# Optimization experiments

Hardware: AMD Instinct MI355X
Metric: run time of the kernel (lower is better)

Reference implementation:

```python
import jax, jax.numpy as jnp
import numpy as np

N = 1048576   # samples
C = 64        # classes (Y unique targets)
S = 8         # subgroups


def setup_inputs() -> dict:
    key = jax.random.key(0)
    k1, k2, k3 = jax.random.split(key, 3)
    logits = jax.random.normal(k1, (N, C), dtype=jnp.float32)
    targets = jax.random.randint(k2, (N,), 0, C, dtype=jnp.int64)
    subgroup_inf = jax.random.randint(k3, (N,), 0, S, dtype=jnp.int64)
    return {"logits": logits, "targets": targets, "subgroup_inf": subgroup_inf}


def reference(logits, targets, subgroup_inf):
    # per-sample cross-entropy (loss_fn with reduction='none')
    logp = jax.nn.log_softmax(logits, axis=-1)                       # [N, C]
    per_sample = -jnp.take_along_axis(logp, targets[:, None], axis=-1)[:, 0]  # [N]

    # composite (target, subgroup) key -> group counts via one scatter-add
    key_ids = targets * S + subgroup_inf                              # [N]
    counts = jax.ops.segment_sum(jnp.ones_like(per_sample), key_ids,
                                 num_segments=C * S)                  # [C*S]
    # every sample's own group has count >= 1, so no div-by-zero
    weighted = per_sample / counts[key_ids]
    return jnp.sum(weighted)
```

## Files before the change

### kernel.cpp

```cpp
#include <hip/hip_runtime.h>


#define NKEYS 512
#define NSLICES 512
typedef float v4f __attribute__((ext_vector_type(4)));

__device__ __forceinline__ float pick4(v4f v, int j) {
    float r = v.x;
    r = (j == 1) ? v.y : r;
    r = (j == 2) ? v.z : r;
    r = (j == 3) ? v.w : r;
    return r;
}

__device__ __forceinline__ float esum4(v4f v) {
    return __expf(v.x) + __expf(v.y) + __expf(v.z) + __expf(v.w);
}

__global__ __launch_bounds__(256)
void orl_hist_kernel(const float* __restrict__ logits,
                     const int* __restrict__ targets,
                     const int* __restrict__ subg,
                     float* __restrict__ psum,
                     unsigned int* __restrict__ pcnt,
                     int n) {
    __shared__ float        lsum[NKEYS];
    __shared__ unsigned int lcnt[NKEYS];
    for (int i = threadIdx.x; i < NKEYS; i += 256) { lsum[i] = 0.0f; lcnt[i] = 0u; }
    __syncthreads();

    const int lane = threadIdx.x & 63;
    const int q    = lane & 15;
    const int g    = lane >> 4;
    const int wave = (blockIdx.x << 2) | (threadIdx.x >> 6);
    const int nwaves = gridDim.x << 2;

    int base = wave * 16;
    for (; base + 16 <= n; base += nwaves * 16) {
        const int r0 = base + g, r1 = base + 4 + g, r2 = base + 8 + g, r3 = base + 12 + g;
        const v4f v0 = __builtin_nontemporal_load((const v4f*)(logits + (size_t)r0 * 64) + q);
        const v4f v1 = __builtin_nontemporal_load((const v4f*)(logits + (size_t)r1 * 64) + q);
        const v4f v2 = __builtin_nontemporal_load((const v4f*)(logits + (size_t)r2 * 64) + q);
        const v4f v3 = __builtin_nontemporal_load((const v4f*)(logits + (size_t)r3 * 64) + q);
        const int t0 = targets[r0], t1 = targets[r1], t2 = targets[r2], t3 = targets[r3];
        const int u0 = subg[r0],    u1 = subg[r1],    u2 = subg[r2],    u3 = subg[r3];

        float s0 = esum4(v0), s1 = esum4(v1), s2 = esum4(v2), s3 = esum4(v3);
        #pragma unroll
        for (int m = 1; m < 16; m <<= 1) {
            s0 += __shfl_xor(s0, m, 16);
            s1 += __shfl_xor(s1, m, 16);
            s2 += __shfl_xor(s2, m, 16);
            s3 += __shfl_xor(s3, m, 16);
        }
        if ((t0 >> 2) == q) {
            const float ps = __logf(s0) - pick4(v0, t0 & 3);
            atomicAdd(&lsum[t0 * 8 + u0], ps); atomicAdd(&lcnt[t0 * 8 + u0], 1u);
        }
        if ((t1 >> 2) == q) {
            const float ps = __logf(s1) - pick4(v1, t1 & 3);
            atomicAdd(&lsum[t1 * 8 + u1], ps); atomicAdd(&lcnt[t1 * 8 + u1], 1u);
        }
        if ((t2 >> 2) == q) {
            const float ps = __logf(s2) - pick4(v2, t2 & 3);
            atomicAdd(&lsum[t2 * 8 + u2], ps); atomicAdd(&lcnt[t2 * 8 + u2], 1u);
        }
        if ((t3 >> 2) == q) {
            const float ps = __logf(s3) - pick4(v3, t3 & 3);
            atomicAdd(&lsum[t3 * 8 + u3], ps); atomicAdd(&lcnt[t3 * 8 + u3], 1u);
        }
    }
    for (int o = 0; o < 16; o += 4) {
        const int r = base + o + g;
        if (r < n) {
            const v4f v = *((const v4f*)(logits + (size_t)r * 64) + q);
            const int t = targets[r];
            float s = esum4(v);
            #pragma unroll
            for (int m = 1; m < 16; m <<= 1) s += __shfl_xor(s, m, 16);
            if ((t >> 2) == q) {
                const float ps = __logf(s) - pick4(v, t & 3);
                const int key = t * 8 + subg[r];
                atomicAdd(&lsum[key], ps); atomicAdd(&lcnt[key], 1u);
            }
        }
    }

    __syncthreads();
    const size_t sbase = (size_t)blockIdx.x * NKEYS;
    for (int i = threadIdx.x; i < NKEYS; i += 256) {
        psum[sbase + i] = lsum[i];
        pcnt[sbase + i] = lcnt[i];
    }
}

__global__ __launch_bounds__(1024)
void orl_reduce_kernel(const float* __restrict__ psum,
                       const unsigned int* __restrict__ pcnt,
                       float* __restrict__ out) {
    const int t = threadIdx.x;
    const int k = t & (NKEYS - 1);
    const int h = t >> 9;
    float s = 0.0f; unsigned int c = 0u;
    const int b0 = h * (NSLICES / 2);
    #pragma unroll 8
    for (int b = b0; b < b0 + NSLICES / 2; ++b) {
        s += psum[(size_t)b * NKEYS + k];
        c += pcnt[(size_t)b * NKEYS + k];
    }
    __shared__ float        s2[NKEYS];
    __shared__ unsigned int c2[NKEYS];
    if (h) { s2[k] = s; c2[k] = c; }
    __syncthreads();
    float v = 0.0f;
    if (!h) {
        const float S = s + s2[k];
        const unsigned int C = c + c2[k];
        v = C ? S / (float)C : 0.0f;
    }
    #pragma unroll
    for (int m = 32; m > 0; m >>= 1) v += __shfl_down(v, m, 64);
    __shared__ float wred[16];
    if ((t & 63) == 0) wred[t >> 6] = v;
    __syncthreads();
    if (t == 0) {
        float r = 0.0f;
        #pragma unroll
        for (int w = 0; w < 16; ++w) r += wred[w];
        out[0] = r;
    }
}

extern "C" void kernel_launch(void* const* d_in, const int* in_sizes, int n_in,
                              void* d_out, int out_size, void* d_ws, size_t ws_size,
                              hipStream_t stream) {
    const float* logits  = (const float*)d_in[0];
    const int*   targets = (const int*)d_in[1];
    const int*   subg    = (const int*)d_in[2];
    const int n = in_sizes[1];
    float* out = (float*)d_out;

    float*        psum = (float*)d_ws;
    unsigned int* pcnt = (unsigned int*)((char*)d_ws + (size_t)NSLICES * NKEYS * 4);

    orl_hist_kernel<<<NSLICES, 256, 0, stream>>>(logits, targets, subg, psum, pcnt, n);
    orl_reduce_kernel<<<1, 1024, 0, stream>>>(psum, pcnt, out);
}
```

Measured before the change: 373.2 us.

## Vectorize target/subgroup loads and spread final reduction over 64 blocks

In the histogram kernel, each 16-lane group now handles four consecutive rows, so targets and subgroups come in with one int4 load each instead of scalar loads. The logits loads also become per-row contiguous for each group. The reduce kernel moves from a single 1024-thread block to 64 blocks of 256 threads, each summing 8 keys across slices, with shuffle and shared reductions and a final atomicAdd into an output zeroed by a memset. This targets the serial single-block reduce and the scattered index loads, at the cost of an extra memset launch and nondeterministic float atomic ordering.

```diff
diff --git a/kernel.cpp b/kernel.cpp
--- a/kernel.cpp
+++ b/kernel.cpp
@@ -37,13 +37,14 @@
 
     int base = wave * 16;
     for (; base + 16 <= n; base += nwaves * 16) {
-        const int r0 = base + g, r1 = base + 4 + g, r2 = base + 8 + g, r3 = base + 12 + g;
-        const v4f v0 = __builtin_nontemporal_load((const v4f*)(logits + (size_t)r0 * 64) + q);
-        const v4f v1 = __builtin_nontemporal_load((const v4f*)(logits + (size_t)r1 * 64) + q);
-        const v4f v2 = __builtin_nontemporal_load((const v4f*)(logits + (size_t)r2 * 64) + q);
-        const v4f v3 = __builtin_nontemporal_load((const v4f*)(logits + (size_t)r3 * 64) + q);
-        const int t0 = targets[r0], t1 = targets[r1], t2 = targets[r2], t3 = targets[r3];
-        const int u0 = subg[r0],    u1 = subg[r1],    u2 = subg[r2],    u3 = subg[r3];
+        const int r0 = base + g * 4;
+        const int4 t4 = *(const int4*)(targets + r0);
+        const int4 u4 = *(const int4*)(subg + r0);
+        const float* rowp = logits + (size_t)r0 * 64 + q * 4;
+        const v4f v0 = __builtin_nontemporal_load((const v4f*)(rowp));
+        const v4f v1 = __builtin_nontemporal_load((const v4f*)(rowp + 64));
+        const v4f v2 = __builtin_nontemporal_load((const v4f*)(rowp + 128));
+        const v4f v3 = __builtin_nontemporal_load((const v4f*)(rowp + 192));
 
         float s0 = esum4(v0), s1 = esum4(v1), s2 = esum4(v2), s3 = esum4(v3);
         #pragma unroll
@@ -53,25 +54,25 @@
             s2 += __shfl_xor(s2, m, 16);
             s3 += __shfl_xor(s3, m, 16);
         }
-        if ((t0 >> 2) == q) {
-            const float ps = __logf(s0) - pick4(v0, t0 & 3);
-            atomicAdd(&lsum[t0 * 8 + u0], ps); atomicAdd(&lcnt[t0 * 8 + u0], 1u);
+        if ((t4.x >> 2) == q) {
+            const float ps = __logf(s0) - pick4(v0, t4.x & 3);
+            atomicAdd(&lsum[t4.x * 8 + u4.x], ps); atomicAdd(&lcnt[t4.x * 8 + u4.x], 1u);
         }
-        if ((t1 >> 2) == q) {
-            const float ps = __logf(s1) - pick4(v1, t1 & 3);
-            atomicAdd(&lsum[t1 * 8 + u1], ps); atomicAdd(&lcnt[t1 * 8 + u1], 1u);
+        if ((t4.y >> 2) == q) {
+            const float ps = __logf(s1) - pick4(v1, t4.y & 3);
+            atomicAdd(&lsum[t4.y * 8 + u4.y], ps); atomicAdd(&lcnt[t4.y * 8 + u4.y], 1u);
         }
-        if ((t2 >> 2) == q) {
-            const float ps = __logf(s2) - pick4(v2, t2 & 3);
-            atomicAdd(&lsum[t2 * 8 + u2], ps); atomicAdd(&lcnt[t2 * 8 + u2], 1u);
+        if ((t4.z >> 2) == q) {
+            const float ps = __logf(s2) - pick4(v2, t4.z & 3);
+            atomicAdd(&lsum[t4.z * 8 + u4.z], ps); atomicAdd(&lcnt[t4.z * 8 + u4.z], 1u);
         }
-        if ((t3 >> 2) == q) {
-            const float ps = __logf(s3) - pick4(v3, t3 & 3);
-            atomicAdd(&lsum[t3 * 8 + u3], ps); atomicAdd(&lcnt[t3 * 8 + u3], 1u);
+        if ((t4.w >> 2) == q) {
+            const float ps = __logf(s3) - pick4(v3, t4.w & 3);
+            atomicAdd(&lsum[t4.w * 8 + u4.w], ps); atomicAdd(&lcnt[t4.w * 8 + u4.w], 1u);
         }
     }
-    for (int o = 0; o < 16; o += 4) {
-        const int r = base + o + g;
+    for (int o = 0; o < 4; ++o) {
+        const int r = base + g * 4 + o;
         if (r < n) {
             const v4f v = *((const v4f*)(logits + (size_t)r * 64) + q);
             const int t = targets[r];
@@ -94,40 +95,36 @@
     }
 }
 
-__global__ __launch_bounds__(1024)
+__global__ __launch_bounds__(256)
 void orl_reduce_kernel(const float* __restrict__ psum,
                        const unsigned int* __restrict__ pcnt,
                        float* __restrict__ out) {
-    const int t = threadIdx.x;
-    const int k = t & (NKEYS - 1);
-    const int h = t >> 9;
+    const int kk  = threadIdx.x & 7;
+    const int sl  = threadIdx.x >> 3;
+    const int key = (blockIdx.x << 3) | kk;
     float s = 0.0f; unsigned int c = 0u;
-    const int b0 = h * (NSLICES / 2);
-    #pragma unroll 8
-    for (int b = b0; b < b0 + NSLICES / 2; ++b) {
-        s += psum[(size_t)b * NKEYS + k];
-        c += pcnt[(size_t)b * NKEYS + k];
-    }
-    __shared__ float        s2[NKEYS];
-    __shared__ unsigned int c2[NKEYS];
-    if (h) { s2[k] = s; c2[k] = c; }
-    __syncthreads();
-    float v = 0.0f;
-    if (!h) {
-        const float S = s + s2[k];
-        const unsigned int C = c + c2[k];
-        v = C ? S / (float)C : 0.0f;
+    #pragma unroll 4
+    for (int b = sl; b < NSLICES; b += 32) {
+        s += psum[(size_t)b * NKEYS + key];
+        c += pcnt[(size_t)b * NKEYS + key];
     }
     #pragma unroll
-    for (int m = 32; m > 0; m >>= 1) v += __shfl_down(v, m, 64);
-    __shared__ float wred[16];
-    if ((t & 63) == 0) wred[t >> 6] = v;
+    for (int m = 8; m < 64; m <<= 1) {
+        s += __shfl_xor(s, m, 64);
+        c += __shfl_xor(c, m, 64);
+    }
+    __shared__ float        ls[4][8];
+    __shared__ unsigned int lc[4][8];
+    const int w = threadIdx.x >> 6;
+    if ((threadIdx.x & 63) < 8) { ls[w][kk] = s; lc[w][kk] = c; }
     __syncthreads();
-    if (t == 0) {
-        float r = 0.0f;
+    if (threadIdx.x < 8) {
+        const float        S = ls[0][kk] + ls[1][kk] + ls[2][kk] + ls[3][kk];
+        const unsigned int C = lc[0][kk] + lc[1][kk] + lc[2][kk] + lc[3][kk];
+        float v = C ? S / (float)C : 0.0f;
         #pragma unroll
-        for (int w = 0; w < 16; ++w) r += wred[w];
-        out[0] = r;
+        for (int m = 1; m < 8; m <<= 1) v += __shfl_xor(v, m, 8);
+        if (threadIdx.x == 0) atomicAdd(out, v);
     }
 }
 
@@ -143,6 +140,7 @@
     float*        psum = (float*)d_ws;
     unsigned int* pcnt = (unsigned int*)((char*)d_ws + (size_t)NSLICES * NKEYS * 4);
 
+    hipMemsetAsync(out, 0, sizeof(float), stream);
     orl_hist_kernel<<<NSLICES, 256, 0, stream>>>(logits, targets, subg, psum, pcnt, n);
-    orl_reduce_kernel<<<1, 1024, 0, stream>>>(psum, pcnt, out);
+    orl_reduce_kernel<<<64, 256, 0, stream>>>(psum, pcnt, out);
 }
```

Measured after the change: 361.0 us. 1.03x faster.
